# Optimization experiments

Measured on AMD Instinct MI355X. Metric: run time of the kernel, lower is better.

The kernel has to match this reference:

```python
import jax, jax.numpy as jnp
import numpy as np

N_NODES = 50000
N_EDGES = 800000
IN_CH = 128
HEADS = 4
OUT_CH = 4
N_GRAPHS = 64
NEG_SLOPE = 0.2  # GATv2Conv default leaky_relu slope
EPS = 1e-5       # GraphNorm eps


def _seg_sum(x, seg, n):
    return jax.ops.segment_sum(x, seg, num_segments=n)


def _seg_mean(x, seg, n):
    s = _seg_sum(x, seg, n)
    cnt = _seg_sum(jnp.ones((seg.shape[0],), x.dtype), seg, n)
    return s / jnp.maximum(cnt, 1.0)[:, None]


def gatv2_conv(x, src, dst, n, w_l, w_r, att, bias, heads, out_ch, concat):
    # x: [N, F_in]; src/dst: [E_tot] (self-loops already appended)
    x_l = (x @ w_l).reshape(n, heads, out_ch)
    x_r = (x @ w_r).reshape(n, heads, out_ch)
    m = jax.nn.leaky_relu(x_l[src] + x_r[dst], NEG_SLOPE)   # [E, H, C]
    e = jnp.einsum('ehc,hc->eh', m, att)                    # [E, H]
    # softmax over incoming edges of each destination node
    e_max = jax.ops.segment_max(e, dst, num_segments=n)     # [N, H]
    w = jnp.exp(e - e_max[dst])
    denom = _seg_sum(w, dst, n)                             # [N, H]
    alpha = w / denom[dst]
    out = _seg_sum(alpha[:, :, None] * x_l[src], dst, n)    # [N, H, C]
    out = out.reshape(n, heads * out_ch) if concat else out.mean(axis=1)
    return out + bias


def graph_norm(x, batch, weight, bias, mean_scale, n_graphs):
    mu = _seg_mean(x, batch, n_graphs)                      # [G, C]
    out = x - mu[batch] * mean_scale
    var = _seg_mean(out * out, batch, n_graphs)
    return out / jnp.sqrt(var[batch] + EPS) * weight + bias


def setup_inputs() -> dict:
    key = jax.random.key(0)
    ks = jax.random.split(key, 20)
    H = HEADS
    d = {}
    d['x'] = jax.random.normal(ks[0], (N_NODES, IN_CH), dtype=jnp.float32)
    d['edge_index'] = jax.random.randint(ks[1], (2, N_EDGES), 0, N_NODES, dtype=jnp.int32)
    d['batch'] = jnp.sort(jax.random.randint(ks[2], (N_NODES,), 0, N_GRAPHS, dtype=jnp.int32))
    def glorot(k, shape):
        fan = shape[0] + shape[-1]
        return jax.random.normal(k, shape, dtype=jnp.float32) * np.sqrt(2.0 / fan).astype(np.float32)
    # layer 1: in 128 -> 32 per head, concat -> 128
    d['w_l1'] = glorot(ks[3], (IN_CH, H * 32)); d['w_r1'] = glorot(ks[4], (IN_CH, H * 32))
    d['att1'] = glorot(ks[5], (H, 32)); d['b1'] = jnp.zeros((H * 32,), jnp.float32)
    d['gn1_w'] = jnp.ones((H * 32,), jnp.float32); d['gn1_b'] = jnp.zeros((H * 32,), jnp.float32); d['gn1_s'] = jnp.ones((H * 32,), jnp.float32)
    # layer 2: 128 -> 16 per head, concat -> 64
    d['w_l2'] = glorot(ks[6], (H * 32, H * 16)); d['w_r2'] = glorot(ks[7], (H * 32, H * 16))
    d['att2'] = glorot(ks[8], (H, 16)); d['b2'] = jnp.zeros((H * 16,), jnp.float32)
    d['gn2_w'] = jnp.ones((H * 16,), jnp.float32); d['gn2_b'] = jnp.zeros((H * 16,), jnp.float32); d['gn2_s'] = jnp.ones((H * 16,), jnp.float32)
    # layer 3: 64 -> 8 per head, mean over heads -> 8
    d['w_l3'] = glorot(ks[9], (H * 16, H * 8)); d['w_r3'] = glorot(ks[10], (H * 16, H * 8))
    d['att3'] = glorot(ks[11], (H, 8)); d['b3'] = jnp.zeros((8,), jnp.float32)
    d['gn3_w'] = jnp.ones((8,), jnp.float32); d['gn3_b'] = jnp.zeros((8,), jnp.float32); d['gn3_s'] = jnp.ones((8,), jnp.float32)
    d['lin_w'] = glorot(ks[12], (8, OUT_CH)); d['lin_b'] = jnp.zeros((OUT_CH,), jnp.float32)
    return d


def reference(x, edge_index, batch,
              w_l1, w_r1, att1, b1, gn1_w, gn1_b, gn1_s,
              w_l2, w_r2, att2, b2, gn2_w, gn2_b, gn2_s,
              w_l3, w_r3, att3, b3, gn3_w, gn3_b, gn3_s,
              lin_w, lin_b):
    n = x.shape[0]
    loop = jnp.arange(n, dtype=edge_index.dtype)
    src = jnp.concatenate([edge_index[0], loop])  # add_self_loops=True (PyG default)
    dst = jnp.concatenate([edge_index[1], loop])
    h = gatv2_conv(x, src, dst, n, w_l1, w_r1, att1, b1, HEADS, 32, True)
    h = jax.nn.relu(graph_norm(h, batch, gn1_w, gn1_b, gn1_s, N_GRAPHS))
    h = gatv2_conv(h, src, dst, n, w_l2, w_r2, att2, b2, HEADS, 16, True)
    h = jax.nn.relu(graph_norm(h, batch, gn2_w, gn2_b, gn2_s, N_GRAPHS))
    h = gatv2_conv(h, src, dst, n, w_l3, w_r3, att3, b3, HEADS, 8, False)
    h = jax.nn.relu(graph_norm(h, batch, gn3_w, gn3_b, gn3_s, N_GRAPHS))
    features = _seg_mean(h, batch, N_GRAPHS)  # global_mean_pool -> [G, 8]
    logits = features @ lin_w + lin_b         # [G, OUT_CH]
    return (logits, features)
```

## Files before the change

### kernel.cpp

```cpp
#include <hip/hip_runtime.h>
#include <hip/hip_fp16.h>
#include <math.h>

#define NN 50000
#define NE 800000
#define ET (NE + NN)
#define NG 64
#define H 4
#define NBK 196
#define CH 4096
#define SB ((ET + CH - 1) / CH)

typedef _Float16 half8 __attribute__((ext_vector_type(8)));
typedef _Float16 hv2 __attribute__((ext_vector_type(2)));
typedef float floatx4 __attribute__((ext_vector_type(4)));


__device__ __forceinline__ void edge_sd(int e, const int* __restrict__ ei, int& s, int& d) {
    if (e < NE) { s = ei[e]; d = ei[NE + e]; } else { s = e - NE; d = s; }
}

__global__ __launch_bounds__(256) void k_bhist(const int* __restrict__ ei, int* __restrict__ bcnt) {
    __shared__ int hist[NBK];
    int b0 = blockIdx.x, tid = threadIdx.x;
    for (int i = tid; i < NBK; i += 256) hist[i] = 0;
    __syncthreads();
#pragma unroll
    for (int pass = 0; pass < CH / 256; ++pass) {
        int e = b0 * CH + pass * 256 + tid;
        if (e < ET) {
            int d = (e < NE) ? ei[NE + e] : (e - NE);
            atomicAdd(&hist[d >> 8], 1);
        }
    }
    __syncthreads();
    if (tid < NBK) bcnt[tid * SB + b0] = hist[tid];
}

__global__ __launch_bounds__(256) void k_bscanA(const int* __restrict__ bcnt, int* __restrict__ boff,
                                                int* __restrict__ tot) {
    __shared__ int lds[256];
    int b = blockIdx.x, t = threadIdx.x;
    int v = (t < SB) ? bcnt[b * SB + t] : 0;
    lds[t] = v;
    __syncthreads();
    for (int off = 1; off < 256; off <<= 1) {
        int y = (t >= off) ? lds[t - off] : 0;
        __syncthreads();
        lds[t] += y;
        __syncthreads();
    }
    if (t < SB) boff[b * SB + t] = lds[t] - v;
    if (t == 255) tot[b] = lds[255];
}

__global__ __launch_bounds__(256) void k_bscanB(const int* __restrict__ tot, int* __restrict__ ebase,
                                                const int* __restrict__ bpos, int* __restrict__ cnt) {
    __shared__ int lds[256];
    int t = threadIdx.x;
    int v = (t < NBK) ? tot[t] : 0;
    lds[t] = v;
    __syncthreads();
    for (int off = 1; off < 256; off <<= 1) {
        int y = (t >= off) ? lds[t - off] : 0;
        __syncthreads();
        lds[t] += y;
        __syncthreads();
    }
    if (t < NBK) ebase[t] = lds[t] - v;
    if (t == 0) ebase[NBK] = ET;
    if (t < NG) cnt[t] = bpos[t + 1] - bpos[t];
}

__global__ __launch_bounds__(256) void k_bounds(const int* __restrict__ batch, int* __restrict__ bpos) {
    int i = blockIdx.x * 256 + threadIdx.x;
    if (i >= NN) return;
    int cur = batch[i];
    int prev = (i == 0) ? -1 : batch[i - 1];
    for (int g = prev + 1; g <= cur; ++g) bpos[g] = i;
    if (i == NN - 1)
        for (int g = cur + 1; g <= NG; ++g) bpos[g] = NN;
}

__global__ __launch_bounds__(256) void k_bscatter(const int* __restrict__ ei, const int* __restrict__ ebase,
                                                  const int* __restrict__ boff, unsigned int* __restrict__ ebuf) {
    __shared__ int cur[NBK];
    int b0 = blockIdx.x, tid = threadIdx.x;
    for (int i = tid; i < NBK; i += 256) cur[i] = ebase[i] + boff[i * SB + b0];
    __syncthreads();
#pragma unroll
    for (int pass = 0; pass < CH / 256; ++pass) {
        int e = b0 * CH + pass * 256 + tid;
        if (e < ET) {
            int s, d;
            edge_sd(e, ei, s, d);
            int pos = atomicAdd(&cur[d >> 8], 1);
            ebuf[pos] = ((unsigned)s << 16) | (unsigned)(d & 255);
        }
    }
}

__global__ __launch_bounds__(256) void k_bsort(const unsigned int* __restrict__ ebuf,
                                               const int* __restrict__ ebase,
                                               int* __restrict__ rowptr, unsigned short* __restrict__ colsrc) {
    __shared__ int cnt2[256];
    __shared__ int sc[256];
    __shared__ int cur2[256];
    int b = blockIdx.x, t = threadIdx.x;
    int base = ebase[b], n = ebase[b + 1] - base;
    cnt2[t] = 0;
    __syncthreads();
    for (int i = t; i < n; i += 256) atomicAdd(&cnt2[ebuf[base + i] & 255], 1);
    __syncthreads();
    int v = cnt2[t];
    sc[t] = v;
    __syncthreads();
    for (int off = 1; off < 256; off <<= 1) {
        int y = (t >= off) ? sc[t - off] : 0;
        __syncthreads();
        sc[t] += y;
        __syncthreads();
    }
    int excl = sc[t] - v;
    int d = b * 256 + t;
    if (d < NN) rowptr[d] = base + excl;
    if (b == 0 && t == 0) rowptr[NN] = ET;
    cur2[t] = excl;
    __syncthreads();
    for (int i = t; i < n; i += 256) {
        unsigned u = ebuf[base + i];
        int pos = atomicAdd(&cur2[u & 255], 1);
        colsrc[base + pos] = (unsigned short)(u >> 16);
    }
}


__global__ __launch_bounds__(256) void k_cast(const float* __restrict__ x, __half* __restrict__ xh) {
    int i = blockIdx.x * 256 + threadIdx.x;
    size_t base = (size_t)i * 8;
    if (base >= (size_t)NN * 128) return;
    const float4* p = (const float4*)(x + base);
    float4 a = p[0], b = p[1];
    half8 h;
    h[0] = (_Float16)a.x; h[1] = (_Float16)a.y; h[2] = (_Float16)a.z; h[3] = (_Float16)a.w;
    h[4] = (_Float16)b.x; h[5] = (_Float16)b.y; h[6] = (_Float16)b.z; h[7] = (_Float16)b.w;
    *(half8*)(xh + base) = h;
}


template <int K, int M2>
__device__ __forceinline__ void wprep_fn(int chunk, const float* __restrict__ Wl, const float* __restrict__ Wr,
                                         _Float16* __restrict__ Wfrag) {
    constexpr int MTOT = 2 * M2, NT = MTOT / 16;
    if (chunk >= MTOT * K / 8) return;
    int lane = chunk & 63, tt = chunk >> 6;
    int t = tt % NT, kt = tt / NT;
    int n = t * 16 + (lane & 15);
    int kb = kt * 32 + (lane >> 4) * 8;
    const float* src = (n < M2) ? (Wl + n) : (Wr + (n - M2));
    half8 h;
#pragma unroll
    for (int j = 0; j < 8; ++j) h[j] = (_Float16)src[(size_t)(kb + j) * M2];
    *(half8*)(Wfrag + (size_t)chunk * 8) = h;
}

__global__ __launch_bounds__(256) void k_wprep_all(const float* __restrict__ Wl1, const float* __restrict__ Wr1,
                                                   const float* __restrict__ Wl2, const float* __restrict__ Wr2,
                                                   const float* __restrict__ Wl3, const float* __restrict__ Wr3,
                                                   _Float16* __restrict__ Wf1, _Float16* __restrict__ Wf2,
                                                   _Float16* __restrict__ Wf3) {
    int b = blockIdx.x, t = threadIdx.x;
    if (b < 16)      wprep_fn<128, 128>(b * 256 + t, Wl1, Wr1, Wf1);
    else if (b < 24) wprep_fn<128, 64>((b - 16) * 256 + t, Wl2, Wr2, Wf2);
    else             wprep_fn<64, 32>((b - 24) * 256 + t, Wl3, Wr3, Wf3);
}


template <int K, int M2>
__global__ __launch_bounds__(256) void k_dualgemm(const __half* __restrict__ Ain,
                                                  const _Float16* __restrict__ Wfrag,
                                                  __half* __restrict__ Ol, float* __restrict__ Or) {
    constexpr int MTOT = 2 * M2;
    constexpr int NT = MTOT / 16;
    constexpr int KT = K / 32;
    int tid = threadIdx.x;
    int wid = tid >> 6, lane = tid & 63;
    int q = lane >> 4, l15 = lane & 15;
    int r0 = blockIdx.x * 64 + wid * 16;
    int arow = min(r0 + l15, NN - 1);
    const _Float16* A = (const _Float16*)Ain;
    const _Float16* ap = A + (size_t)arow * K + q * 8;

    floatx4 acc[NT];
#pragma unroll
    for (int t = 0; t < NT; ++t) acc[t] = (floatx4){0.f, 0.f, 0.f, 0.f};

#pragma unroll
    for (int kt = 0; kt < KT; ++kt) {
        half8 a8 = *(const half8*)(ap + kt * 32);
        const _Float16* wp = Wfrag + ((size_t)(kt * NT) * 64 + lane) * 8;
#pragma unroll
        for (int t = 0; t < NT; ++t) {
            half8 b8 = *(const half8*)(wp + (size_t)t * 64 * 8);
            acc[t] = __builtin_amdgcn_mfma_f32_16x16x32_f16(a8, b8, acc[t], 0, 0, 0);
        }
    }

#pragma unroll
    for (int t = 0; t < NT; ++t) {
        int cn = t * 16 + l15;
#pragma unroll
        for (int reg = 0; reg < 4; ++reg) {
            int r = r0 + q * 4 + reg;
            if (r < NN) {
                if (cn < M2) Ol[(size_t)r * M2 + cn] = __float2half(acc[t][reg]);
                else         Or[(size_t)r * M2 + (cn - M2)] = acc[t][reg];
            }
        }
    }
}


template <int CP> struct HVec { hv2 h2[CP / 2]; };

template <int CP>
__device__ __forceinline__ HVec<CP> load_hv(const __half* __restrict__ p) {
    HVec<CP> r;
    if constexpr (CP == 8) { float4 t = *(const float4*)p; r = *(HVec<CP>*)&t; }
    else if constexpr (CP == 4) { float2 t = *(const float2*)p; r = *(HVec<CP>*)&t; }
    else { r.h2[0] = *(const hv2*)p; }
    return r;
}

template <int C, int EP, bool CONCAT>
__global__ __launch_bounds__(256, 8) void k_attn(const __half* __restrict__ xl, const float* __restrict__ xr,
                                                 const int* __restrict__ rowptr,
                                                 const unsigned short* __restrict__ colsrc,
                                                 const float* __restrict__ att, const float* __restrict__ bias,
                                                 float* __restrict__ out) {
    constexpr int CP = C / EP;
    int t = blockIdx.x * 256 + threadIdx.x;
    int part = t & (EP - 1);
    int nh = t >> 2;
    if (nh >= NN * H) return;
    int node = nh >> 2, h = nh & 3;
    int cbase = h * C + part * CP;
    hv2 xrr2[CP / 2], attv2[CP / 2];
    float acc[CP];
    {
        const float* p = xr + (size_t)node * (H * C) + cbase;
        const float* q = att + cbase;
#pragma unroll
        for (int j = 0; j < CP / 2; ++j) {
            xrr2[j] = (hv2){(_Float16)p[2 * j], (_Float16)p[2 * j + 1]};
            attv2[j] = (hv2){(_Float16)q[2 * j], (_Float16)q[2 * j + 1]};
        }
#pragma unroll
        for (int c = 0; c < CP; ++c) acc[c] = 0.f;
    }
    float denom = 0.f;
    int beg = rowptr[node], end = rowptr[node + 1];

    auto process = [&](const HVec<CP>& xv) {
        float part_s = 0.f;
#pragma unroll
        for (int j = 0; j < CP / 2; ++j) {
            hv2 z = xv.h2[j] + xrr2[j];
            hv2 l = __builtin_elementwise_max(z, z * (_Float16)0.2f);
            part_s = __builtin_amdgcn_fdot2(l, attv2[j], part_s, false);
        }
        float score = part_s;
#pragma unroll
        for (int mask = 1; mask < EP; mask <<= 1) score += __shfl_xor(score, mask, 64);
        float w = __expf(score);
        denom += w;
        const _Float16* xh = (const _Float16*)&xv;
#pragma unroll
        for (int c = 0; c < CP; ++c) acc[c] = fmaf(w, (float)xh[c], acc[c]);
    };

    int idx = beg;
    for (; idx + 2 <= end; idx += 2) {
        int s0 = colsrc[idx], s1 = colsrc[idx + 1];
        HVec<CP> xv0 = load_hv<CP>(xl + (size_t)s0 * (H * C) + cbase);
        HVec<CP> xv1 = load_hv<CP>(xl + (size_t)s1 * (H * C) + cbase);
        process(xv0);
        process(xv1);
    }
    if (idx < end) {
        int s = colsrc[idx];
        HVec<CP> xv = load_hv<CP>(xl + (size_t)s * (H * C) + cbase);
        process(xv);
    }

    float inv = 1.f / denom;
    float* op = out + (size_t)node * (H * C) + cbase;
    float v[CP];
#pragma unroll
    for (int c = 0; c < CP; ++c) {
        v[c] = acc[c] * inv;
        if (CONCAT) v[c] += bias[cbase + c];
    }
    if constexpr (CP == 8) {
        *(float4*)(op) = make_float4(v[0], v[1], v[2], v[3]);
        *(float4*)(op + 4) = make_float4(v[4], v[5], v[6], v[7]);
    } else if constexpr (CP == 4) {
        *(float4*)(op) = make_float4(v[0], v[1], v[2], v[3]);
    } else {
        *(float2*)(op) = make_float2(v[0], v[1]);
    }
}


template <int LOGC, int SPLIT>
__global__ __launch_bounds__(256) void k_gnred2(const float* __restrict__ h, const int* __restrict__ bpos,
                                                float* __restrict__ sum, float* __restrict__ sumsq) {
    constexpr int C = 1 << LOGC;
    constexpr int RG = 256 >> LOGC;
    int g = blockIdx.x / SPLIT, s = blockIdx.x % SPLIT;
    int c = threadIdx.x & (C - 1);
    int rg = threadIdx.x >> LOGC;
    int b0 = bpos[g], b1 = bpos[g + 1];
    int n = b1 - b0;
    int seg = (n + SPLIT - 1) / SPLIT;
    int r0 = b0 + s * seg;
    int r1 = min(r0 + seg, b1);
    float sv = 0.f, ssv = 0.f;
    for (int r = r0 + rg; r < r1; r += RG) {
        float x = h[(size_t)r * C + c];
        sv += x; ssv += x * x;
    }
    __shared__ float ls[256], lss[256];
    ls[threadIdx.x] = sv; lss[threadIdx.x] = ssv;
    __syncthreads();
    for (int off = 128; off >= C; off >>= 1) {
        if (threadIdx.x < off) {
            ls[threadIdx.x] += ls[threadIdx.x + off];
            lss[threadIdx.x] += lss[threadIdx.x + off];
        }
        __syncthreads();
    }
    if (threadIdx.x < C) {
        atomicAdd(&sum[g * C + threadIdx.x], ls[threadIdx.x]);
        atomicAdd(&sumsq[g * C + threadIdx.x], lss[threadIdx.x]);
    }
}

__global__ __launch_bounds__(256) void k_gnnorm(float* __restrict__ h, const int* __restrict__ batch,
                                                const float* __restrict__ sum, const float* __restrict__ sumsq,
                                                const int* __restrict__ cnt, const float* __restrict__ w,
                                                const float* __restrict__ b, const float* __restrict__ ms,
                                                int logC, __half* __restrict__ h16) {
    int C = 1 << logC;
    int i = blockIdx.x * 256 + threadIdx.x;
    if (i >= NN * C) return;
    int nd = i >> logC, c = i & (C - 1);
    int g = batch[nd];
    float cg = fmaxf((float)cnt[g], 1.f);
    float mu = sum[g * C + c] / cg;
    float ex2 = sumsq[g * C + c] / cg;
    float s_ = ms[c];
    float var = ex2 - (2.f * s_ - s_ * s_) * mu * mu;
    float y = (h[i] - mu * s_) * rsqrtf(var + 1e-5f) * w[c] + b[c];
    y = fmaxf(y, 0.f);
    h[i] = y;
    if (h16) h16[i] = __float2half(y);
}


template <int SPLIT>
__global__ __launch_bounds__(256) void k_headgn(const float* __restrict__ tmp, const float* __restrict__ b3,
                                                const int* __restrict__ bpos, float* __restrict__ Af,
                                                float* __restrict__ sum, float* __restrict__ sumsq) {
    constexpr int C = 8, RG = 32;
    int g = blockIdx.x / SPLIT, s = blockIdx.x % SPLIT;
    int c = threadIdx.x & 7;
    int rg = threadIdx.x >> 3;
    int b0 = bpos[g], b1 = bpos[g + 1];
    int n = b1 - b0;
    int seg = (n + SPLIT - 1) / SPLIT;
    int r0 = b0 + s * seg;
    int r1 = min(r0 + seg, b1);
    float bias = b3[c];
    float sv = 0.f, ssv = 0.f;
    for (int r = r0 + rg; r < r1; r += RG) {
        const float* p = tmp + (size_t)r * 32 + c;
        float v = 0.25f * (p[0] + p[8] + p[16] + p[24]) + bias;
        Af[(size_t)r * C + c] = v;
        sv += v; ssv += v * v;
    }
    __shared__ float ls[256], lss[256];
    ls[threadIdx.x] = sv; lss[threadIdx.x] = ssv;
    __syncthreads();
    for (int off = 128; off >= C; off >>= 1) {
        if (threadIdx.x < off) {
            ls[threadIdx.x] += ls[threadIdx.x + off];
            lss[threadIdx.x] += lss[threadIdx.x + off];
        }
        __syncthreads();
    }
    if (threadIdx.x < C) {
        atomicAdd(&sum[g * C + threadIdx.x], ls[threadIdx.x]);
        atomicAdd(&sumsq[g * C + threadIdx.x], lss[threadIdx.x]);
    }
}


template <int SPLIT>
__global__ __launch_bounds__(256) void k_gnpool(float* __restrict__ Af, const int* __restrict__ bpos,
                                                const float* __restrict__ sum, const float* __restrict__ sumsq,
                                                const int* __restrict__ cnt, const float* __restrict__ w,
                                                const float* __restrict__ b, const float* __restrict__ ms,
                                                float* __restrict__ pool) {
    constexpr int C = 8, RG = 32;
    int g = blockIdx.x / SPLIT, s = blockIdx.x % SPLIT;
    int c = threadIdx.x & 7;
    int rg = threadIdx.x >> 3;
    int b0 = bpos[g], b1 = bpos[g + 1];
    int n = b1 - b0;
    int seg = (n + SPLIT - 1) / SPLIT;
    int r0 = b0 + s * seg;
    int r1 = min(r0 + seg, b1);
    float cg = fmaxf((float)cnt[g], 1.f);
    float mu = sum[g * C + c] / cg;
    float ex2 = sumsq[g * C + c] / cg;
    float s_ = ms[c];
    float var = ex2 - (2.f * s_ - s_ * s_) * mu * mu;
    float rs = rsqrtf(var + 1e-5f) * w[c];
    float bb = b[c], mus = mu * s_;
    float pv = 0.f;
    for (int r = r0 + rg; r < r1; r += RG) {
        size_t i = (size_t)r * C + c;
        float y = fmaxf((Af[i] - mus) * rs + bb, 0.f);
        Af[i] = y;
        pv += y;
    }
    __shared__ float ls[256];
    ls[threadIdx.x] = pv;
    __syncthreads();
    for (int off = 128; off >= C; off >>= 1) {
        if (threadIdx.x < off) ls[threadIdx.x] += ls[threadIdx.x + off];
        __syncthreads();
    }
    if (threadIdx.x < C) atomicAdd(&pool[g * C + threadIdx.x], ls[threadIdx.x]);
}


__global__ __launch_bounds__(512) void k_final(const float* __restrict__ pool, const int* __restrict__ cnt,
                                               const float* __restrict__ lw, const float* __restrict__ lb,
                                               float* __restrict__ outp) {
    __shared__ float feat[512];
    int t = threadIdx.x;
    int g = t >> 3;
    float f = pool[t] / fmaxf((float)cnt[g], 1.f);
    feat[t] = f;
    outp[256 + t] = f;
    __syncthreads();
    if (t < 256) {
        int g2 = t >> 2, o = t & 3;
        float a = lb[o];
#pragma unroll
        for (int cc = 0; cc < 8; ++cc) a += feat[g2 * 8 + cc] * lw[cc * 4 + o];
        outp[t] = a;
    }
}


extern "C" void kernel_launch(void* const* d_in, const int* in_sizes, int n_in,
                              void* d_out, int out_size, void* d_ws, size_t ws_size,
                              hipStream_t stream) {
    const float* x    = (const float*)d_in[0];
    const int*   ei   = (const int*)d_in[1];
    const int*   batch= (const int*)d_in[2];
    const float *w_l1 = (const float*)d_in[3],  *w_r1 = (const float*)d_in[4];
    const float *att1 = (const float*)d_in[5],  *b1   = (const float*)d_in[6];
    const float *gn1w = (const float*)d_in[7],  *gn1b = (const float*)d_in[8],  *gn1s = (const float*)d_in[9];
    const float *w_l2 = (const float*)d_in[10], *w_r2 = (const float*)d_in[11];
    const float *att2 = (const float*)d_in[12], *b2   = (const float*)d_in[13];
    const float *gn2w = (const float*)d_in[14], *gn2b = (const float*)d_in[15], *gn2s = (const float*)d_in[16];
    const float *w_l3 = (const float*)d_in[17], *w_r3 = (const float*)d_in[18];
    const float *att3 = (const float*)d_in[19], *b3   = (const float*)d_in[20];
    const float *gn3w = (const float*)d_in[21], *gn3b = (const float*)d_in[22], *gn3s = (const float*)d_in[23];
    const float *lw   = (const float*)d_in[24], *lb   = (const float*)d_in[25];

    char* ws = (char*)d_ws;
    size_t off = 0;
    auto alloc = [&](size_t bytes) -> void* {
        void* p = ws + off;
        off += (bytes + 255) & ~(size_t)255;
        return p;
    };
    __half* Ah  = (__half*)alloc((size_t)NN * 128 * 2);
    __half* Xh  = (__half*)alloc((size_t)NN * 128 * 2);
    float*  B   = (float*)alloc((size_t)NN * 128 * 4);
    float*  Cb  = (float*)alloc((size_t)NN * 64 * 4);
    float*  Af  = (float*)alloc((size_t)NN * 8 * 4);
    _Float16* Wf1 = (_Float16*)alloc((size_t)256 * 128 * 2);
    _Float16* Wf2 = (_Float16*)alloc((size_t)128 * 128 * 2);
    _Float16* Wf3 = (_Float16*)alloc((size_t)64 * 64 * 2);
    int* rowptr = (int*)alloc((size_t)(NN + 1) * 4);
    unsigned short* colsrc = (unsigned short*)alloc((size_t)ET * 2);
    unsigned int* ebuf = (unsigned int*)alloc((size_t)ET * 4);
    int* bcnt   = (int*)alloc((size_t)NBK * SB * 4);
    int* boff   = (int*)alloc((size_t)NBK * SB * 4);
    int* tot    = (int*)alloc((size_t)NBK * 4);
    int* ebase  = (int*)alloc((size_t)(NBK + 1) * 4);
    int* bpos   = (int*)alloc((size_t)(NG + 1) * 4);
    int* cnt    = (int*)alloc((size_t)NG * 4);
    char* zbase = ws + off;
    float* sum1 = (float*)alloc((size_t)NG * 128 * 4);
    float* sq1  = (float*)alloc((size_t)NG * 128 * 4);
    float* sum2 = (float*)alloc((size_t)NG * 64 * 4);
    float* sq2  = (float*)alloc((size_t)NG * 64 * 4);
    float* sum3 = (float*)alloc((size_t)NG * 8 * 4);
    float* sq3  = (float*)alloc((size_t)NG * 8 * 4);
    float* pool = (float*)alloc((size_t)NG * 8 * 4);
    size_t zbytes = (size_t)((ws + off) - zbase);
    (void)hipMemsetAsync(zbase, 0, zbytes, stream);

    k_cast<<<(NN * 128 / 8 + 255) / 256, 256, 0, stream>>>(x, Xh);
    k_wprep_all<<<26, 256, 0, stream>>>(w_l1, w_r1, w_l2, w_r2, w_l3, w_r3, Wf1, Wf2, Wf3);
    k_bounds<<<(NN + 255) / 256, 256, 0, stream>>>(batch, bpos);
    k_bhist<<<SB, 256, 0, stream>>>(ei, bcnt);
    k_bscanA<<<NBK, 256, 0, stream>>>(bcnt, boff, tot);
    k_bscanB<<<1, 256, 0, stream>>>(tot, ebase, bpos, cnt);
    k_bscatter<<<SB, 256, 0, stream>>>(ei, ebase, boff, ebuf);
    k_bsort<<<NBK, 256, 0, stream>>>(ebuf, ebase, rowptr, colsrc);

    int gA4 = (NN * H * 4) / 256;
    int gD  = (NN + 63) / 64;

    k_dualgemm<128, 128><<<gD, 256, 0, stream>>>(Xh, Wf1, Ah, B);
    k_attn<32, 4, true><<<gA4, 256, 0, stream>>>(Ah, B, rowptr, colsrc, att1, b1, B);
    k_gnred2<7, 8><<<NG * 8, 256, 0, stream>>>(B, bpos, sum1, sq1);
    k_gnnorm<<<(NN * 128 + 255) / 256, 256, 0, stream>>>(B, batch, sum1, sq1, cnt, gn1w, gn1b, gn1s, 7, Xh);

    k_dualgemm<128, 64><<<gD, 256, 0, stream>>>(Xh, Wf2, Ah, Cb);
    k_attn<16, 4, true><<<gA4, 256, 0, stream>>>(Ah, Cb, rowptr, colsrc, att2, b2, Cb);
    k_gnred2<6, 8><<<NG * 8, 256, 0, stream>>>(Cb, bpos, sum2, sq2);
    k_gnnorm<<<(NN * 64 + 255) / 256, 256, 0, stream>>>(Cb, batch, sum2, sq2, cnt, gn2w, gn2b, gn2s, 6, Xh);

    k_dualgemm<64, 32><<<gD, 256, 0, stream>>>(Xh, Wf3, Ah, B);
    k_attn<8, 4, false><<<gA4, 256, 0, stream>>>(Ah, B, rowptr, colsrc, att3, nullptr, B);
    k_headgn<8><<<NG * 8, 256, 0, stream>>>(B, b3, bpos, Af, sum3, sq3);
    k_gnpool<8><<<NG * 8, 256, 0, stream>>>(Af, bpos, sum3, sq3, cnt, gn3w, gn3b, gn3s, pool);
    k_final<<<1, 512, 0, stream>>>(pool, cnt, lw, lb, (float*)d_out);
}
```

Baseline: 355.2 us.

## Fuse input cast into first GEMM, unroll attention gather, drop dead stores

Removes the separate fp32-to-fp16 cast kernel by having the first dual GEMM load fp32 rows and convert them in registers. Unrolls the attention edge loop from 2 to 4 gathers per iteration so more independent loads are in flight. Also drops the fp32 write-back in GraphNorm when an fp16 copy is produced, and the unused write-back in the final pooled norm. This saves a launch and several full-tensor writes, at the cost of more register pressure in the attention kernel.

```diff
diff --git a/kernel.cpp b/kernel.cpp
--- a/kernel.cpp
+++ b/kernel.cpp
@@ -132,19 +132,6 @@
         int pos = atomicAdd(&cur2[u & 255], 1);
         colsrc[base + pos] = (unsigned short)(u >> 16);
     }
-}
-
-
-__global__ __launch_bounds__(256) void k_cast(const float* __restrict__ x, __half* __restrict__ xh) {
-    int i = blockIdx.x * 256 + threadIdx.x;
-    size_t base = (size_t)i * 8;
-    if (base >= (size_t)NN * 128) return;
-    const float4* p = (const float4*)(x + base);
-    float4 a = p[0], b = p[1];
-    half8 h;
-    h[0] = (_Float16)a.x; h[1] = (_Float16)a.y; h[2] = (_Float16)a.z; h[3] = (_Float16)a.w;
-    h[4] = (_Float16)b.x; h[5] = (_Float16)b.y; h[6] = (_Float16)b.z; h[7] = (_Float16)b.w;
-    *(half8*)(xh + base) = h;
 }
 
 
@@ -176,8 +163,22 @@
 }
 
 
-template <int K, int M2>
-__global__ __launch_bounds__(256) void k_dualgemm(const __half* __restrict__ Ain,
+template <typename AT>
+__device__ __forceinline__ half8 load_a8(const AT* __restrict__ ap) {
+    if constexpr (__is_same(AT, _Float16)) {
+        return *(const half8*)ap;
+    } else {
+        const float4* p = (const float4*)ap;
+        float4 a = p[0], b = p[1];
+        half8 h;
+        h[0] = (_Float16)a.x; h[1] = (_Float16)a.y; h[2] = (_Float16)a.z; h[3] = (_Float16)a.w;
+        h[4] = (_Float16)b.x; h[5] = (_Float16)b.y; h[6] = (_Float16)b.z; h[7] = (_Float16)b.w;
+        return h;
+    }
+}
+
+template <int K, int M2, typename AT>
+__global__ __launch_bounds__(256) void k_dualgemm(const AT* __restrict__ Ain,
                                                   const _Float16* __restrict__ Wfrag,
                                                   __half* __restrict__ Ol, float* __restrict__ Or) {
     constexpr int MTOT = 2 * M2;
@@ -188,8 +189,7 @@
     int q = lane >> 4, l15 = lane & 15;
     int r0 = blockIdx.x * 64 + wid * 16;
     int arow = min(r0 + l15, NN - 1);
-    const _Float16* A = (const _Float16*)Ain;
-    const _Float16* ap = A + (size_t)arow * K + q * 8;
+    const AT* ap = Ain + (size_t)arow * K + q * 8;
 
     floatx4 acc[NT];
 #pragma unroll
@@ -197,7 +197,7 @@
 
 #pragma unroll
     for (int kt = 0; kt < KT; ++kt) {
-        half8 a8 = *(const half8*)(ap + kt * 32);
+        half8 a8 = load_a8<AT>(ap + kt * 32);
         const _Float16* wp = Wfrag + ((size_t)(kt * NT) * 64 + lane) * 8;
 #pragma unroll
         for (int t = 0; t < NT; ++t) {
@@ -280,14 +280,18 @@
     };
 
     int idx = beg;
-    for (; idx + 2 <= end; idx += 2) {
-        int s0 = colsrc[idx], s1 = colsrc[idx + 1];
+    for (; idx + 4 <= end; idx += 4) {
+        int s0 = colsrc[idx], s1 = colsrc[idx + 1], s2 = colsrc[idx + 2], s3 = colsrc[idx + 3];
         HVec<CP> xv0 = load_hv<CP>(xl + (size_t)s0 * (H * C) + cbase);
         HVec<CP> xv1 = load_hv<CP>(xl + (size_t)s1 * (H * C) + cbase);
+        HVec<CP> xv2 = load_hv<CP>(xl + (size_t)s2 * (H * C) + cbase);
+        HVec<CP> xv3 = load_hv<CP>(xl + (size_t)s3 * (H * C) + cbase);
         process(xv0);
         process(xv1);
-    }
-    if (idx < end) {
+        process(xv2);
+        process(xv3);
+    }
+    for (; idx < end; ++idx) {
         int s = colsrc[idx];
         HVec<CP> xv = load_hv<CP>(xl + (size_t)s * (H * C) + cbase);
         process(xv);
@@ -363,8 +367,8 @@
     float var = ex2 - (2.f * s_ - s_ * s_) * mu * mu;
     float y = (h[i] - mu * s_) * rsqrtf(var + 1e-5f) * w[c] + b[c];
     y = fmaxf(y, 0.f);
-    h[i] = y;
     if (h16) h16[i] = __float2half(y);
+    else     h[i] = y;
 }
 
 
@@ -407,7 +411,7 @@
 
 
 template <int SPLIT>
-__global__ __launch_bounds__(256) void k_gnpool(float* __restrict__ Af, const int* __restrict__ bpos,
+__global__ __launch_bounds__(256) void k_gnpool(const float* __restrict__ Af, const int* __restrict__ bpos,
                                                 const float* __restrict__ sum, const float* __restrict__ sumsq,
                                                 const int* __restrict__ cnt, const float* __restrict__ w,
                                                 const float* __restrict__ b, const float* __restrict__ ms,
@@ -430,9 +434,7 @@
     float bb = b[c], mus = mu * s_;
     float pv = 0.f;
     for (int r = r0 + rg; r < r1; r += RG) {
-        size_t i = (size_t)r * C + c;
-        float y = fmaxf((Af[i] - mus) * rs + bb, 0.f);
-        Af[i] = y;
+        float y = fmaxf((Af[(size_t)r * C + c] - mus) * rs + bb, 0.f);
         pv += y;
     }
     __shared__ float ls[256];
@@ -518,7 +520,6 @@
     size_t zbytes = (size_t)((ws + off) - zbase);
     (void)hipMemsetAsync(zbase, 0, zbytes, stream);
 
-    k_cast<<<(NN * 128 / 8 + 255) / 256, 256, 0, stream>>>(x, Xh);
     k_wprep_all<<<26, 256, 0, stream>>>(w_l1, w_r1, w_l2, w_r2, w_l3, w_r3, Wf1, Wf2, Wf3);
     k_bounds<<<(NN + 255) / 256, 256, 0, stream>>>(batch, bpos);
     k_bhist<<<SB, 256, 0, stream>>>(ei, bcnt);
@@ -530,17 +531,17 @@
     int gA4 = (NN * H * 4) / 256;
     int gD  = (NN + 63) / 64;
 
-    k_dualgemm<128, 128><<<gD, 256, 0, stream>>>(Xh, Wf1, Ah, B);
+    k_dualgemm<128, 128, float><<<gD, 256, 0, stream>>>(x, Wf1, Ah, B);
     k_attn<32, 4, true><<<gA4, 256, 0, stream>>>(Ah, B, rowptr, colsrc, att1, b1, B);
     k_gnred2<7, 8><<<NG * 8, 256, 0, stream>>>(B, bpos, sum1, sq1);
     k_gnnorm<<<(NN * 128 + 255) / 256, 256, 0, stream>>>(B, batch, sum1, sq1, cnt, gn1w, gn1b, gn1s, 7, Xh);
 
-    k_dualgemm<128, 64><<<gD, 256, 0, stream>>>(Xh, Wf2, Ah, Cb);
+    k_dualgemm<128, 64, _Float16><<<gD, 256, 0, stream>>>((const _Float16*)Xh, Wf2, Ah, Cb);
     k_attn<16, 4, true><<<gA4, 256, 0, stream>>>(Ah, Cb, rowptr, colsrc, att2, b2, Cb);
     k_gnred2<6, 8><<<NG * 8, 256, 0, stream>>>(Cb, bpos, sum2, sq2);
     k_gnnorm<<<(NN * 64 + 255) / 256, 256, 0, stream>>>(Cb, batch, sum2, sq2, cnt, gn2w, gn2b, gn2s, 6, Xh);
 
-    k_dualgemm<64, 32><<<gD, 256, 0, stream>>>(Xh, Wf3, Ah, B);
+    k_dualgemm<64, 32, _Float16><<<gD, 256, 0, stream>>>((const _Float16*)Xh, Wf3, Ah, B);
     k_attn<8, 4, false><<<gA4, 256, 0, stream>>>(Ah, B, rowptr, colsrc, att3, nullptr, B);
     k_headgn<8><<<NG * 8, 256, 0, stream>>>(B, b3, bpos, Af, sum3, sq3);
     k_gnpool<8><<<NG * 8, 256, 0, stream>>>(Af, bpos, sum3, sq3, cnt, gn3w, gn3b, gn3s, pool);
```

New measurement: 336.3 us. 1.06x faster.
